# Kernel optimization log

Measured on AMD Instinct MI355X. Metric: run time of the kernel, lower is better.

## Reference

```python
import jax, jax.numpy as jnp
import numpy as np

T = 4096          # num tokens
HID = 2048        # hidden_size
HQ = 32           # num q heads
HKV = 8           # num kv heads
G = HQ // HKV     # GQA group size
D = 128           # head_dim (q/k)
DV = 96           # v_head_dim
W = 512           # sliding window (= query block size)
THETA = 1e6
Q_SIZE, K_SIZE, V_SIZE = HQ * D, HKV * D, HKV * DV


def setup_inputs() -> dict:
    key = jax.random.key(0)
    k1, k2, k3, k4 = jax.random.split(key, 4)
    positions = jnp.arange(T, dtype=jnp.int32)
    hidden_states = jax.random.normal(k1, (T, HID), dtype=jnp.float32)
    qkv_w = jax.random.normal(k2, (Q_SIZE + K_SIZE + V_SIZE, HID), dtype=jnp.float32) * (HID ** -0.5)
    o_w = jax.random.normal(k3, (HID, HQ * DV), dtype=jnp.float32) * ((HQ * DV) ** -0.5)
    sink_bias = jax.random.normal(k4, (HQ,), dtype=jnp.float32)
    return {"positions": positions, "hidden_states": hidden_states,
            "qkv_w": qkv_w, "o_w": o_w, "sink_bias": sink_bias}


def _rope(x, positions):
    # neox-style rotate-half RoPE on full head_dim (partial_rotary_factor=1.0)
    half = D // 2
    inv_freq = 1.0 / (THETA ** (jnp.arange(0, half, dtype=jnp.float32) / half))
    ang = positions.astype(jnp.float32)[:, None] * inv_freq[None, :]   # [T, D/2]
    cos = jnp.cos(ang)[:, None, :]
    sin = jnp.sin(ang)[:, None, :]
    x1, x2 = x[..., :half], x[..., half:]
    return jnp.concatenate([x1 * cos - x2 * sin, x2 * cos + x1 * sin], axis=-1)


def _swa_with_sink(q, k, v, sink_bias):
    # q: [T, HKV, G, D], k: [T, HKV, D], v: [T, HKV, DV]
    nb = T // W
    scale = D ** -0.5
    qb = q.reshape(nb, W, HKV, G, D)
    # per query block i, keys/values from global span [(i-1)*W, (i+1)*W)
    k_pad = jnp.pad(k, ((W, 0), (0, 0), (0, 0)))
    v_pad = jnp.pad(v, ((W, 0), (0, 0), (0, 0)))
    idx = jnp.arange(nb)[:, None] * W + jnp.arange(2 * W)[None, :]     # [nb, 2W]
    k_ext = k_pad[idx]                                                 # [nb, 2W, HKV, D]
    v_ext = v_pad[idx]                                                 # [nb, 2W, HKV, DV]
    # mask: rel = t - j in [0, W); exclude left-pad keys (key_pos < 0)
    r = jnp.arange(W)[:, None]
    c = jnp.arange(2 * W)[None, :]
    rel = W + r - c                                                    # [W, 2W]
    key_pos = (jnp.arange(nb)[:, None, None] - 1) * W + c[None]        # [nb, W(1), 2W]
    mask = (rel >= 0) & (rel < W) & (key_pos >= 0)                     # [nb, W, 2W]
    scores = jnp.einsum('nrkgd,nckd->nkgrc', qb, k_ext) * scale        # [nb,HKV,G,W,2W]
    scores = jnp.where(mask[:, None, None, :, :], scores, -jnp.inf)
    sink = jnp.broadcast_to(sink_bias.reshape(HKV, G)[None, :, :, None, None],
                            (nb, HKV, G, W, 1))
    logits = jnp.concatenate([scores, sink], axis=-1)                  # [...,2W+1]
    p = jax.nn.softmax(logits, axis=-1)[..., :-1]                      # drop sink column
    out = jnp.einsum('nkgrc,nckd->nrkgd', p, v_ext)                    # [nb,W,HKV,G,DV]
    return out.reshape(T, HQ * DV)


def reference(positions, hidden_states, qkv_w, o_w, sink_bias):
    qkv = hidden_states @ qkv_w.T                                      # [T, Q+K+V]
    q, k, v = jnp.split(qkv, [Q_SIZE, Q_SIZE + K_SIZE], axis=-1)
    q = q.reshape(T, HQ, D)
    k = k.reshape(T, HKV, D)
    v = v.reshape(T, HKV, DV)
    q = _rope(q, positions).reshape(T, HKV, G, D)
    k = _rope(k, positions)
    attn = _swa_with_sink(q, k, v, sink_bias)                          # [T, HQ*DV]
    return attn @ o_w.T                                                # [T, HID]
```

## Files before the change

kernel.cpp:

```cpp
#include <hip/hip_runtime.h>
#include <hip/hip_bf16.h>
#include <stdint.h>

#define T_SEQ 4096
#define HIDDEN 2048
#define NQH 32
#define NKVH 8
#define DH 128
#define DVH 96
#define WWIN 512
#define QKVN 5888
#define KOFF 4096
#define VOFF 5120
#define ATTN 3072
#define QSCALE 0.08838834764831845f

typedef uint16_t u16;
typedef uint32_t u32;
typedef __bf16 bfrag8 __attribute__((ext_vector_type(8)));
typedef float f32x4v __attribute__((ext_vector_type(4)));
typedef float f32x16 __attribute__((ext_vector_type(16)));

__device__ __forceinline__ u16 f2bf(float x) {
  u32 u = __float_as_uint(x);
  return (u16)((u + 0x7fffu + ((u >> 16) & 1u)) >> 16);
}
__device__ __forceinline__ float bf2f(u16 v) { return __uint_as_float(((u32)v) << 16); }

__device__ __forceinline__ void gload16(const u16* src, char* ldst) {
  __builtin_amdgcn_global_load_lds((const __attribute__((address_space(1))) u32*)src,
                                   (__attribute__((address_space(3))) u32*)ldst, 16, 0, 0);
}

__global__ void cvt_kernel(const float* __restrict__ in, u16* __restrict__ out, int n4) {
  int i = blockIdx.x * blockDim.x + threadIdx.x;
  int st = gridDim.x * blockDim.x;
  for (; i < n4; i += st) {
    float4 v = ((const float4*)in)[i];
    ushort4 o;
    o.x = f2bf(v.x); o.y = f2bf(v.y); o.z = f2bf(v.z); o.w = f2bf(v.w);
    ((ushort4*)out)[i] = o;
  }
}

template<int OUT_F32>
__global__ __launch_bounds__(512, 2) void gemm_v3(const u16* __restrict__ A,
                                                  const u16* __restrict__ B,
                                                  void* __restrict__ Cp,
                                                  int M, int N, int K, int nbm) {
  extern __shared__ char lds[];
  const int tid = threadIdx.x;
  const int w = tid >> 6, lane = tid & 63;
  const int wr = w >> 1, wc = w & 1;
  const int r5 = lane & 31, kg = lane >> 5;

  const int nwg = gridDim.x;
  int bid = (int)blockIdx.x;
  if ((nwg & 7) == 0) bid = (bid & 7) * (nwg >> 3) + (bid >> 3);
  const int bm = (bid % nbm) * 256;
  const int bn = (bid / nbm) * 128;
  const int NT = K >> 6;

  f32x16 acc[2][2];
#pragma unroll
  for (int mb = 0; mb < 2; mb++)
#pragma unroll
    for (int nb = 0; nb < 2; nb++)
#pragma unroll
      for (int i = 0; i < 16; i++) acc[mb][nb][i] = 0.f;

  const int q = r5 * 128 + ((kg ^ (r5 & 7)) << 4);

  auto stageA = [&](int t) {
    char* dst = lds + (t % 3) * 49152;
    const u16* Abase = A + (size_t)bm * K + ((size_t)t << 6);
#pragma unroll
    for (int i = 0; i < 4; i++) {
      int D = (w * 4 + i) * 1024 + lane * 16;
      int row = D >> 7;
      int kb = (D ^ ((row & 7) << 4)) & 127;
      gload16(Abase + (size_t)row * K + (kb >> 1), dst + D);
    }
  };
  auto stageB = [&](int t) {
    char* dst = lds + (t % 3) * 49152 + 32768;
    const u16* Bbase = B + (size_t)bn * K + ((size_t)t << 6);
#pragma unroll
    for (int i = 0; i < 2; i++) {
      int D = (w * 2 + i) * 1024 + lane * 16;
      int row = D >> 7;
      int kb = (D ^ ((row & 7) << 4)) & 127;
      gload16(Bbase + (size_t)row * K + (kb >> 1), dst + D);
    }
  };

  stageA(0); stageB(0);

  for (int t = 0; t < NT; ++t) {
    const char* Ab = lds + (t % 3) * 49152 + wr * 8192;
    const char* Bb = lds + (t % 3) * 49152 + 32768 + wc * 8192;
    if (t + 1 < NT) {
      stageA(t + 1);
      stageB(t + 1);
      asm volatile("s_waitcnt vmcnt(6)");
    } else {
      asm volatile("s_waitcnt vmcnt(0)");
    }
    asm volatile("s_barrier" ::: "memory");

    bfrag8 af[2][2], bf[2][2];
#pragma unroll
    for (int ks = 0; ks < 2; ks++) {
#pragma unroll
      for (int mb = 0; mb < 2; mb++)
        af[mb][ks] = *(const bfrag8*)(Ab + mb * 4096 + (q ^ (ks << 5)));
#pragma unroll
      for (int nb = 0; nb < 2; nb++)
        bf[nb][ks] = *(const bfrag8*)(Bb + nb * 4096 + (q ^ (ks << 5)));
    }
    __builtin_amdgcn_s_setprio(1);
#pragma unroll
    for (int ks = 0; ks < 2; ks++)
#pragma unroll
      for (int mb = 0; mb < 2; mb++)
#pragma unroll
        for (int nb = 0; nb < 2; nb++)
          acc[mb][nb] = __builtin_amdgcn_mfma_f32_32x32x16_bf16(af[mb][ks], bf[nb][ks], acc[mb][nb], 0, 0, 0);
    __builtin_amdgcn_s_setprio(0);

    bfrag8 af2[2][2], bf2[2][2];
#pragma unroll
    for (int ks = 0; ks < 2; ks++) {
#pragma unroll
      for (int mb = 0; mb < 2; mb++)
        af2[mb][ks] = *(const bfrag8*)(Ab + mb * 4096 + (q ^ ((ks + 2) << 5)));
#pragma unroll
      for (int nb = 0; nb < 2; nb++)
        bf2[nb][ks] = *(const bfrag8*)(Bb + nb * 4096 + (q ^ ((ks + 2) << 5)));
    }
    __builtin_amdgcn_s_setprio(1);
#pragma unroll
    for (int ks = 0; ks < 2; ks++)
#pragma unroll
      for (int mb = 0; mb < 2; mb++)
#pragma unroll
        for (int nb = 0; nb < 2; nb++)
          acc[mb][nb] = __builtin_amdgcn_mfma_f32_32x32x16_bf16(af2[mb][ks], bf2[nb][ks], acc[mb][nb], 0, 0, 0);
    __builtin_amdgcn_s_setprio(0);
  }

  const int rb0 = bm + wr * 64;
  const int cb0 = bn + wc * 64;
#pragma unroll
  for (int mb = 0; mb < 2; mb++)
#pragma unroll
    for (int nb = 0; nb < 2; nb++)
#pragma unroll
      for (int i = 0; i < 16; i++) {
        int rowl = (i & 3) + 8 * (i >> 2) + 4 * kg;
        size_t off = (size_t)(rb0 + mb * 32 + rowl) * N + cb0 + nb * 32 + r5;
        if (OUT_F32) ((float*)Cp)[off] = acc[mb][nb][i];
        else         ((u16*)Cp)[off] = f2bf(acc[mb][nb][i]);
      }
}

template<int OUT_F32>
__global__ __launch_bounds__(256) void gemm_nt(const u16* __restrict__ A,
                                               const u16* __restrict__ B,
                                               void* __restrict__ Cp,
                                               int M, int N, int K) {
  __shared__ u16 Asm[128 * 32];
  __shared__ u16 Bsm[128 * 32];
  const int tid = threadIdx.x;
  const int wv = tid >> 6, lane = tid & 63;
  const int bm = blockIdx.x * 128, bn = blockIdx.y * 128;
  const int wm = (wv >> 1) * 64, wn = (wv & 1) * 64;
  const int srow = lane >> 2;
  const int scol = (lane & 3) * 8;
  const int fr = lane & 15, fk = (lane >> 4) * 8;
  f32x4v acc[4][4];
#pragma unroll
  for (int i = 0; i < 4; i++)
#pragma unroll
    for (int j = 0; j < 4; j++) acc[i][j] = {0.f, 0.f, 0.f, 0.f};

  for (int kt = 0; kt < K; kt += 32) {
    __syncthreads();
#pragma unroll
    for (int c = 0; c < 2; c++) {
      const int ci = wv * 2 + c;
      const u16* ga = A + (size_t)(bm + ci * 16 + srow) * K + kt + scol;
      const u16* gb = B + (size_t)(bn + ci * 16 + srow) * K + kt + scol;
      gload16(ga, (char*)(Asm + ci * 512));
      gload16(gb, (char*)(Bsm + ci * 512));
    }
    __syncthreads();
    bfrag8 af[4], bf[4];
#pragma unroll
    for (int i = 0; i < 4; i++) af[i] = *(const bfrag8*)(Asm + (wm + i * 16 + fr) * 32 + fk);
#pragma unroll
    for (int j = 0; j < 4; j++) bf[j] = *(const bfrag8*)(Bsm + (wn + j * 16 + fr) * 32 + fk);
#pragma unroll
    for (int i = 0; i < 4; i++)
#pragma unroll
      for (int j = 0; j < 4; j++)
        acc[i][j] = __builtin_amdgcn_mfma_f32_16x16x32_bf16(af[i], bf[j], acc[i][j], 0, 0, 0);
  }
  const int orow = (lane >> 4) * 4, ocol = lane & 15;
#pragma unroll
  for (int i = 0; i < 4; i++)
#pragma unroll
    for (int j = 0; j < 4; j++) {
      size_t base = (size_t)(bm + wm + i * 16 + orow) * N + (size_t)(bn + wn + j * 16 + ocol);
#pragma unroll
      for (int r = 0; r < 4; r++) {
        if (OUT_F32) ((float*)Cp)[base + (size_t)r * N] = acc[i][j][r];
        else         ((u16*)Cp)[base + (size_t)r * N] = f2bf(acc[i][j][r]);
      }
    }
}

__global__ void rope_kernel(u16* __restrict__ qkv, const int* __restrict__ pos) {
  int gid = blockIdx.x * 256 + threadIdx.x;
  int d = gid & 63;
  int r = gid >> 6;
  int hh = r % 40;
  int t = r / 40;
  if (t >= T_SEQ) return;
  int off = (hh < 32) ? hh * 128 : KOFF + (hh - 32) * 128;
  u16* p = qkv + (size_t)t * QKVN + off + d;
  float x1 = bf2f(p[0]);
  float x2 = bf2f(p[64]);
  float inv_freq = exp2f(-(float)d * 0.3114307588956852f);
  float ang = (float)pos[t] * inv_freq;
  float c = cosf(ang), s = sinf(ang);
  float y1 = x1 * c - x2 * s;
  float y2 = x2 * c + x1 * s;
  if (hh < 32) { y1 *= QSCALE; y2 *= QSCALE; }
  p[0] = f2bf(y1);
  p[64] = f2bf(y2);
}

__global__ __launch_bounds__(256) void vt_kernel(const u16* __restrict__ qkv,
                                                 u16* __restrict__ vt) {
  __shared__ u16 tile[64][100];
  const int t0 = blockIdx.x * 64;
  const int hk = blockIdx.y;
  const int tid = threadIdx.x;
#pragma unroll
  for (int i = 0; i < 3; i++) {
    int idx = i * 256 + tid;
    int row = idx / 12, ch = idx % 12;
    const u16* g = qkv + (size_t)(t0 + row) * QKVN + VOFF + hk * DVH + ch * 8;
    uint2 a = *(const uint2*)g;
    uint2 b = *(const uint2*)(g + 4);
    *(uint2*)&tile[row][ch * 8] = a;
    *(uint2*)&tile[row][ch * 8 + 4] = b;
  }
  __syncthreads();
#pragma unroll
  for (int i = 0; i < 3; i++) {
    int idx = i * 256 + tid;
    int dv = idx >> 3, tc = (idx & 7) * 8;
    union { uint4 v4; u16 s[8]; } o;
#pragma unroll
    for (int j = 0; j < 8; j++) o.s[j] = tile[tc + j][dv];
    *(uint4*)(vt + (((size_t)(hk * 96 + dv)) << 12) + t0 + tc) = o.v4;
  }
}

__global__ __launch_bounds__(256, 2) void attn_mfma(const u16* __restrict__ qkv,
                                                    const u16* __restrict__ vt,
                                                    const float* __restrict__ sink_bias,
                                                    u16* __restrict__ attn_out) {
  __shared__ u16 k_lds[64 * 128];
  __shared__ u16 v_lds[96 * 64];
  __shared__ u16 p_lds[4][2048];

  const int tid = threadIdx.x;
  const int wv = tid >> 6;
  const int lane = tid & 63;
  const int g = lane >> 4;
  const int c = lane & 15;
  const int t0 = blockIdx.x * 32;
  const int hk = blockIdx.y;
  const int h = hk * 4 + wv;

  bfrag8 qf[2][4];
#pragma unroll
  for (int m = 0; m < 2; m++)
#pragma unroll
    for (int kf = 0; kf < 4; kf++)
      qf[m][kf] = *(const bfrag8*)(qkv + (size_t)(t0 + m * 16 + c) * QKVN + h * DH + kf * 32 + g * 8);

  f32x4v acc_o[2][6];
#pragma unroll
  for (int m = 0; m < 2; m++)
#pragma unroll
    for (int n = 0; n < 6; n++) acc_o[m][n] = {0.f, 0.f, 0.f, 0.f};

  const float sb = sink_bias[h];
  float m_run[2][4], l_run[2][4];
#pragma unroll
  for (int m = 0; m < 2; m++)
#pragma unroll
    for (int r = 0; r < 4; r++) { m_run[m][r] = sb; l_run[m][r] = 1.0f; }

  int cb0 = t0 - (WWIN - 1);
  cb0 = (cb0 < 0) ? 0 : (cb0 & ~63);

  for (int cb = cb0; cb < t0 + 32; cb += 64) {
    __syncthreads();
#pragma unroll
    for (int it = 0; it < 4; it++) {
      int dest = it * 4096 + tid * 16;
      int row = dest >> 8;
      int src = dest ^ ((row & 7) << 4);
      const u16* gp = qkv + (size_t)(cb + row) * QKVN + KOFF + hk * DH + ((src & 255) >> 1);
      gload16(gp, (char*)k_lds + dest);
    }
#pragma unroll
    for (int it = 0; it < 3; it++) {
      int dest = it * 4096 + tid * 16;
      int row = dest >> 7;
      int src = dest ^ ((row & 7) << 4);
      const u16* gp = vt + (((size_t)(hk * 96 + row)) << 12) + cb + ((src & 127) >> 1);
      gload16(gp, (char*)v_lds + dest);
    }
    __syncthreads();

    f32x4v s[2][4];
#pragma unroll
    for (int m = 0; m < 2; m++)
#pragma unroll
      for (int n = 0; n < 4; n++) s[m][n] = {0.f, 0.f, 0.f, 0.f};
#pragma unroll
    for (int kf = 0; kf < 4; kf++) {
      bfrag8 kb[4];
#pragma unroll
      for (int n = 0; n < 4; n++) {
        int key = n * 16 + c;
        int byt = ((key << 8) + (kf << 6) + (g << 4)) ^ ((key & 7) << 4);
        kb[n] = *(const bfrag8*)((const char*)k_lds + byt);
      }
#pragma unroll
      for (int m = 0; m < 2; m++)
#pragma unroll
        for (int n = 0; n < 4; n++)
          s[m][n] = __builtin_amdgcn_mfma_f32_16x16x32_bf16(qf[m][kf], kb[n], s[m][n], 0, 0, 0);
    }

    if ((cb + 63 > t0) || (cb + WWIN < t0 + 32)) {
#pragma unroll
      for (int m = 0; m < 2; m++)
#pragma unroll
        for (int n = 0; n < 4; n++)
#pragma unroll
          for (int r = 0; r < 4; r++) {
            int rel = (t0 + m * 16 + g * 4 + r) - (cb + n * 16 + c);
            if (!(rel >= 0 && rel < WWIN)) s[m][n][r] = -3.0e38f;
          }
    }

    float corr[2][4];
#pragma unroll
    for (int m = 0; m < 2; m++)
#pragma unroll
      for (int r = 0; r < 4; r++) {
        float v0 = fmaxf(fmaxf(s[m][0][r], s[m][1][r]), fmaxf(s[m][2][r], s[m][3][r]));
        v0 = fmaxf(v0, __shfl_xor(v0, 1));
        v0 = fmaxf(v0, __shfl_xor(v0, 2));
        v0 = fmaxf(v0, __shfl_xor(v0, 4));
        v0 = fmaxf(v0, __shfl_xor(v0, 8));
        float mn = fmaxf(m_run[m][r], v0);
        corr[m][r] = __expf(m_run[m][r] - mn);
        m_run[m][r] = mn;
        float p0 = __expf(s[m][0][r] - mn);
        float p1 = __expf(s[m][1][r] - mn);
        float p2 = __expf(s[m][2][r] - mn);
        float p3 = __expf(s[m][3][r] - mn);
        s[m][0][r] = p0; s[m][1][r] = p1; s[m][2][r] = p2; s[m][3][r] = p3;
        float rs = p0 + p1 + p2 + p3;
        rs += __shfl_xor(rs, 1);
        rs += __shfl_xor(rs, 2);
        rs += __shfl_xor(rs, 4);
        rs += __shfl_xor(rs, 8);
        l_run[m][r] = l_run[m][r] * corr[m][r] + rs;
      }
#pragma unroll
    for (int m = 0; m < 2; m++)
#pragma unroll
      for (int n = 0; n < 6; n++)
#pragma unroll
      for (int r = 0; r < 4; r++) acc_o[m][n][r] *= corr[m][r];

#pragma unroll
    for (int m = 0; m < 2; m++)
#pragma unroll
      for (int n = 0; n < 4; n++) {
        u32 lo = (u32)f2bf(s[m][n][0]) | ((u32)f2bf(s[m][n][1]) << 16);
        u32 hi = (u32)f2bf(s[m][n][2]) | ((u32)f2bf(s[m][n][3]) << 16);
        int byt = ((m * 2 + (n >> 1)) << 10) | (g << 3) | ((c & 3) << 5) |
                  (((c >> 2) & 1) << 9) | ((((n & 1) * 2) + (c >> 3)) << 7);
        uint2 u; u.x = lo; u.y = hi;
        *(uint2*)((char*)&p_lds[wv][0] + byt) = u;
      }

#pragma unroll
    for (int ks = 0; ks < 2; ks++) {
      bfrag8 pa[2];
#pragma unroll
      for (int m = 0; m < 2; m++) {
        union { bfrag8 v; u16 s16[8]; } u;
#pragma unroll
        for (int j = 0; j < 4; j++) {
          int e = ((m * 2 + ks) << 9) + c + j * 16 + g * 64;
          u.s16[j] = p_lds[wv][e];
          u.s16[4 + j] = p_lds[wv][e + 256];
        }
        pa[m] = u.v;
      }
#pragma unroll
      for (int n = 0; n < 6; n++) {
        int dv = n * 16 + c;
        int byt = ((dv << 7) + (ks << 6) + (g << 4)) ^ ((dv & 7) << 4);
        bfrag8 vb = *(const bfrag8*)((const char*)v_lds + byt);
#pragma unroll
        for (int m = 0; m < 2; m++)
          acc_o[m][n] = __builtin_amdgcn_mfma_f32_16x16x32_bf16(pa[m], vb, acc_o[m][n], 0, 0, 0);
      }
    }
  }

#pragma unroll
  for (int m = 0; m < 2; m++) {
    float inv[4];
#pragma unroll
    for (int r = 0; r < 4; r++) inv[r] = 1.0f / l_run[m][r];
#pragma unroll
    for (int n = 0; n < 6; n++)
#pragma unroll
      for (int r = 0; r < 4; r++) {
        int tq = t0 + m * 16 + g * 4 + r;
        attn_out[(size_t)tq * ATTN + h * DVH + n * 16 + c] = f2bf(acc_o[m][n][r] * inv[r]);
      }
  }
}

extern "C" void kernel_launch(void* const* d_in, const int* in_sizes, int n_in,
                              void* d_out, int out_size, void* d_ws, size_t ws_size,
                              hipStream_t stream) {
  const int* positions = (const int*)d_in[0];
  const float* hidden = (const float*)d_in[1];
  const float* qkv_w = (const float*)d_in[2];
  const float* o_w = (const float*)d_in[3];
  const float* sink = (const float*)d_in[4];
  char* ws = (char*)d_ws;

  u16* hs_bf   = (u16*)(ws + 0);
  u16* w1_bf   = (u16*)(ws + 16777216);
  u16* attn_bf = (u16*)(ws + 0);
  u16* vt_buf  = (u16*)(ws + 25165824);
  u16* w2_bf   = (u16*)(ws + 40894464);
  u16* qkv_bf  = (u16*)(ws + 53477376);

  bool v3Ok =
    (hipFuncSetAttribute((const void*)&gemm_v3<0>,
                         hipFuncAttributeMaxDynamicSharedMemorySize, 147456) == hipSuccess) &&
    (hipFuncSetAttribute((const void*)&gemm_v3<1>,
                         hipFuncAttributeMaxDynamicSharedMemorySize, 147456) == hipSuccess);

  cvt_kernel<<<dim3(1024), dim3(256), 0, stream>>>(hidden, hs_bf, 8388608 / 4);
  cvt_kernel<<<dim3(1024), dim3(256), 0, stream>>>(qkv_w, w1_bf, 12058624 / 4);
  cvt_kernel<<<dim3(1024), dim3(256), 0, stream>>>(o_w, w2_bf, 6291456 / 4);

  if (v3Ok)
    gemm_v3<0><<<dim3(736), dim3(512), 147456, stream>>>(hs_bf, w1_bf, (void*)qkv_bf,
                                                         T_SEQ, QKVN, HIDDEN, 16);
  else
    gemm_nt<0><<<dim3(32, 46), dim3(256), 0, stream>>>(hs_bf, w1_bf, (void*)qkv_bf,
                                                       T_SEQ, QKVN, HIDDEN);

  rope_kernel<<<dim3(40960), dim3(256), 0, stream>>>(qkv_bf, positions);
  vt_kernel<<<dim3(T_SEQ / 64, NKVH), dim3(256), 0, stream>>>(qkv_bf, vt_buf);
  attn_mfma<<<dim3(T_SEQ / 32, NKVH), dim3(256), 0, stream>>>(qkv_bf, vt_buf, sink, attn_bf);

  if (v3Ok)
    gemm_v3<1><<<dim3(256), dim3(512), 147456, stream>>>(attn_bf, w2_bf, d_out,
                                                         T_SEQ, HIDDEN, ATTN, 16);
  else
    gemm_nt<1><<<dim3(32, 16), dim3(256), 0, stream>>>(attn_bf, w2_bf, d_out,
                                                       T_SEQ, HIDDEN, ATTN);
}
```

Baseline: 312.4 us.

## Double-buffer K/V tiles in attention kernel with async prefetch

Converts the attention kernel's K/V shared-memory tiles into two buffers in dynamic shared memory and prefetches the next two key chunks while computing the current one. Partial vmcnt waits and raw barriers replace the full __syncthreads pair, so global loads overlap with the MFMA work. Shared memory per block grows from about 40KB to 72KB, which can cut occupancy below the launch-bounds target of two blocks per CU. It also relies on the exact count of outstanding loads being correct for the vmcnt(7) wait.

Result: no change. 313.5 us (+0.4%).

```diff
diff --git a/kernel.cpp b/kernel.cpp
--- a/kernel.cpp
+++ b/kernel.cpp
@@ -273,9 +273,7 @@
                                                     const u16* __restrict__ vt,
                                                     const float* __restrict__ sink_bias,
                                                     u16* __restrict__ attn_out) {
-  __shared__ u16 k_lds[64 * 128];
-  __shared__ u16 v_lds[96 * 64];
-  __shared__ u16 p_lds[4][2048];
+  extern __shared__ char smem[];
 
   const int tid = threadIdx.x;
   const int wv = tid >> 6;
@@ -285,6 +283,7 @@
   const int t0 = blockIdx.x * 32;
   const int hk = blockIdx.y;
   const int h = hk * 4 + wv;
+  u16* pw = (u16*)(smem + 57344 + wv * 4096);
 
   bfrag8 qf[2][4];
 #pragma unroll
@@ -308,26 +307,38 @@
 
   int cb0 = t0 - (WWIN - 1);
   cb0 = (cb0 < 0) ? 0 : (cb0 & ~63);
-
-  for (int cb = cb0; cb < t0 + 32; cb += 64) {
-    __syncthreads();
+  const int nc = (t0 + 32 - cb0 + 63) >> 6;
+
+  auto stage = [&](int ci) {
+    const int cb = cb0 + ci * 64;
+    char* kd = smem + (ci & 1) * 16384;
+    char* vd = smem + 32768 + (ci & 1) * 12288;
 #pragma unroll
     for (int it = 0; it < 4; it++) {
       int dest = it * 4096 + tid * 16;
       int row = dest >> 8;
       int src = dest ^ ((row & 7) << 4);
-      const u16* gp = qkv + (size_t)(cb + row) * QKVN + KOFF + hk * DH + ((src & 255) >> 1);
-      gload16(gp, (char*)k_lds + dest);
+      gload16(qkv + (size_t)(cb + row) * QKVN + KOFF + hk * DH + ((src & 255) >> 1), kd + dest);
     }
 #pragma unroll
     for (int it = 0; it < 3; it++) {
       int dest = it * 4096 + tid * 16;
       int row = dest >> 7;
       int src = dest ^ ((row & 7) << 4);
-      const u16* gp = vt + (((size_t)(hk * 96 + row)) << 12) + cb + ((src & 127) >> 1);
-      gload16(gp, (char*)v_lds + dest);
-    }
-    __syncthreads();
+      gload16(vt + (((size_t)(hk * 96 + row)) << 12) + cb + ((src & 127) >> 1), vd + dest);
+    }
+  };
+
+  stage(0);
+  if (nc > 1) stage(1);
+
+  for (int ci = 0; ci < nc; ci++) {
+    const int cb = cb0 + ci * 64;
+    const char* k_lds = smem + (ci & 1) * 16384;
+    const char* v_lds = smem + 32768 + (ci & 1) * 12288;
+    if (ci + 1 < nc) asm volatile("s_waitcnt vmcnt(7)");
+    else             asm volatile("s_waitcnt vmcnt(0)");
+    asm volatile("s_barrier" ::: "memory");
 
     f32x4v s[2][4];
 #pragma unroll
@@ -341,7 +352,7 @@
       for (int n = 0; n < 4; n++) {
         int key = n * 16 + c;
         int byt = ((key << 8) + (kf << 6) + (g << 4)) ^ ((key & 7) << 4);
-        kb[n] = *(const bfrag8*)((const char*)k_lds + byt);
+        kb[n] = *(const bfrag8*)(k_lds + byt);
       }
 #pragma unroll
       for (int m = 0; m < 2; m++)
@@ -403,7 +414,7 @@
         int byt = ((m * 2 + (n >> 1)) << 10) | (g << 3) | ((c & 3) << 5) |
                   (((c >> 2) & 1) << 9) | ((((n & 1) * 2) + (c >> 3)) << 7);
         uint2 u; u.x = lo; u.y = hi;
-        *(uint2*)((char*)&p_lds[wv][0] + byt) = u;
+        *(uint2*)((char*)pw + byt) = u;
       }
 
 #pragma unroll
@@ -415,8 +426,8 @@
 #pragma unroll
         for (int j = 0; j < 4; j++) {
           int e = ((m * 2 + ks) << 9) + c + j * 16 + g * 64;
-          u.s16[j] = p_lds[wv][e];
-          u.s16[4 + j] = p_lds[wv][e + 256];
+          u.s16[j] = pw[e];
+          u.s16[4 + j] = pw[e + 256];
         }
         pa[m] = u.v;
       }
@@ -424,12 +435,15 @@
       for (int n = 0; n < 6; n++) {
         int dv = n * 16 + c;
         int byt = ((dv << 7) + (ks << 6) + (g << 4)) ^ ((dv & 7) << 4);
-        bfrag8 vb = *(const bfrag8*)((const char*)v_lds + byt);
+        bfrag8 vb = *(const bfrag8*)(v_lds + byt);
 #pragma unroll
         for (int m = 0; m < 2; m++)
           acc_o[m][n] = __builtin_amdgcn_mfma_f32_16x16x32_bf16(pa[m], vb, acc_o[m][n], 0, 0, 0);
       }
     }
+
+    asm volatile("s_barrier" ::: "memory");
+    if (ci + 2 < nc) stage(ci + 2);
   }
 
 #pragma unroll
@@ -469,6 +483,9 @@
                          hipFuncAttributeMaxDynamicSharedMemorySize, 147456) == hipSuccess) &&
     (hipFuncSetAttribute((const void*)&gemm_v3<1>,
                          hipFuncAttributeMaxDynamicSharedMemorySize, 147456) == hipSuccess);
+  bool atOk = (hipFuncSetAttribute((const void*)&attn_mfma,
+                 hipFuncAttributeMaxDynamicSharedMemorySize, 73728) == hipSuccess);
+  (void)atOk;
 
   cvt_kernel<<<dim3(1024), dim3(256), 0, stream>>>(hidden, hs_bf, 8388608 / 4);
   cvt_kernel<<<dim3(1024), dim3(256), 0, stream>>>(qkv_w, w1_bf, 12058624 / 4);
@@ -483,7 +500,7 @@
 
   rope_kernel<<<dim3(40960), dim3(256), 0, stream>>>(qkv_bf, positions);
   vt_kernel<<<dim3(T_SEQ / 64, NKVH), dim3(256), 0, stream>>>(qkv_bf, vt_buf);
-  attn_mfma<<<dim3(T_SEQ / 32, NKVH), dim3(256), 0, stream>>>(qkv_bf, vt_buf, sink, attn_bf);
+  attn_mfma<<<dim3(T_SEQ / 32, NKVH), dim3(256), 73728, stream>>>(qkv_bf, vt_buf, sink, attn_bf);
 
   if (v3Ok)
     gemm_v3<1><<<dim3(256), dim3(512), 147456, stream>>>(attn_bf, w2_bf, d_out,
```
